# Kernel optimization log

Hardware: AMD Instinct MI355X
Metric: run time of the kernel (lower is better)

Reference implementation:

```python
import jax, jax.numpy as jnp
import numpy as np

B, S, T = 32, 2048, 768
NH, DH, DHID = 8, 96, 384  # num_heads, head_dim, hidden_dim=4*head_dim


def setup_inputs() -> dict:
    key = jax.random.key(0)
    k = jax.random.split(key, 7)
    token_embeddings = jax.random.normal(k[0], (B, S, T), dtype=jnp.float32)
    attention_mask = jnp.ones((B, S), dtype=jnp.float32)
    # per-head Linear params, stacked on a leading head axis (PyTorch default-ish init scale)
    P_w = jax.random.normal(k[1], (NH, T, DH), dtype=jnp.float32) * (1.0 / np.sqrt(T))
    P_b = jax.random.normal(k[2], (NH, DH), dtype=jnp.float32) * 0.01
    W1_w = jax.random.normal(k[3], (NH, DH, DHID), dtype=jnp.float32) * (1.0 / np.sqrt(DH))
    W1_b = jax.random.normal(k[4], (NH, DHID), dtype=jnp.float32) * 0.01
    W2_w = jax.random.normal(k[5], (NH, DHID, DH), dtype=jnp.float32) * (1.0 / np.sqrt(DHID))
    W2_b = jax.random.normal(k[6], (NH, DH), dtype=jnp.float32) * 0.01
    return {
        'token_embeddings': token_embeddings,
        'attention_mask': attention_mask,
        'P_w': P_w, 'P_b': P_b,
        'W1_w': W1_w, 'W1_b': W1_b,
        'W2_w': W2_w, 'W2_b': W2_b,
    }


def reference(token_embeddings, attention_mask, P_w, P_b, W1_w, W1_b, W2_w, W2_b):
    # Batched over heads instead of the original Python loop; same math per head.
    # H_i = P_i(H): (B, NH, S, DH)
    Hi = jnp.einsum('bst,htd->bhsd', token_embeddings, P_w) + P_b[None, :, None, :]
    # A_i = W2_i(relu(W1_i(H_i))): (B, NH, S, DH)
    A = jax.nn.relu(jnp.einsum('bhsd,hde->bhse', Hi, W1_w) + W1_b[None, :, None, :])
    A = jnp.einsum('bhse,hed->bhsd', A, W2_w) + W2_b[None, :, None, :]
    # masked softmax over the sequence axis (log(mask) adds -inf at padded tokens)
    log_mask = jnp.log(attention_mask)[:, None, :, None]  # (B,1,S,1)
    A = jax.nn.softmax(A + log_mask, axis=2)
    # weighted sum over tokens: (B, NH, DH)
    v = jnp.sum(Hi * A, axis=2)
    # concat heads -> (B, NH*DH) == (B, sentence_dim)
    return v.reshape(v.shape[0], NH * DH)
```

## Files before the change

### kernel.cpp

```cpp
#include <hip/hip_runtime.h>
#include <cstdint>
#include <cstddef>

#define Bsz   32
#define Ssz   2048
#define Tsz   768
#define NH    8
#define DH    96
#define DHID  384
#define Ncols (NH*DH)

using u16 = unsigned short;
typedef __bf16 bf16x8 __attribute__((ext_vector_type(8)));
typedef __bf16 bf16x4 __attribute__((ext_vector_type(4)));
typedef float  f32x4  __attribute__((ext_vector_type(4)));

__device__ __forceinline__ u16 f2bn(float f) {
  __bf16 h = (__bf16)f;
  return __builtin_bit_cast(u16, h);
}
__device__ __forceinline__ float b2f(u16 u) {
  return __builtin_bit_cast(float, (uint32_t)u << 16);
}

__global__ __launch_bounds__(256) void k_pack(const float* __restrict__ Pw,
    const float* __restrict__ W1w, const float* __restrict__ W2w,
    u16* __restrict__ B1t, u16* __restrict__ W1t, u16* __restrict__ W2t)
{
  int i = blockIdx.x * 256 + threadIdx.x;
  if (i < 589824) {
    int n = i / 768, k = i % 768;
    int h = n / 96, d = n % 96;
    B1t[i] = f2bn(Pw[(size_t)h*73728 + (size_t)k*96 + d]);
  } else if (i < 589824 + 294912) {
    int j = i - 589824;
    int h = j / 36864, r = j % 36864;
    int n = r / 96, k = r % 96;
    W1t[j] = f2bn(W1w[(size_t)h*36864 + (size_t)k*384 + n]);
  } else if (i < 589824 + 2*294912) {
    int q = i - 589824 - 294912;
    int h = q / 36864, r = q % 36864;
    int n = r / 384, k = r % 384;
    W2t[q] = f2bn(W2w[(size_t)h*36864 + (size_t)k*96 + n]);
  }
}

__global__ __launch_bounds__(256, 2) void k_gemm1(const float* __restrict__ emb,
    const u16* __restrict__ B1t, const float* __restrict__ Pb, u16* __restrict__ Hi)
{
  __shared__ u16 As[256*64];
  __shared__ u16 Bs[128*64];
  const int tid  = threadIdx.x;
  const int lane = tid & 63;
  const int w    = tid >> 6;
  const int wr = w >> 1, wc = w & 1;
  const int L = blockIdx.x;
  const int widx = (L & 7) * 192 + (L >> 3);
  const int bm = widx / 6, bn = widx % 6;
  const int l15 = lane & 15, lg = lane >> 4;

  const int srow   = lane >> 3;
  const int schunk = lane & 7;
  const int wchunk = schunk ^ srow;

  bf16x8 pa[8];
  bf16x8 pb[4];

  auto load_tile = [&](int kt) {
    const int k0 = kt * 64;
    #pragma unroll
    for (int i = 0; i < 8; ++i) {
      const int row = w*64 + i*8 + srow;
      const float* src = emb + (size_t)(bm*256 + row)*Tsz + k0 + schunk*8;
      float4 v0 = *reinterpret_cast<const float4*>(src);
      float4 v1 = *reinterpret_cast<const float4*>(src + 4);
      bf16x8 af;
      af[0] = (__bf16)v0.x; af[1] = (__bf16)v0.y; af[2] = (__bf16)v0.z; af[3] = (__bf16)v0.w;
      af[4] = (__bf16)v1.x; af[5] = (__bf16)v1.y; af[6] = (__bf16)v1.z; af[7] = (__bf16)v1.w;
      pa[i] = af;
    }
    #pragma unroll
    for (int i = 0; i < 4; ++i) {
      const int row = w*32 + i*8 + srow;
      pb[i] = *reinterpret_cast<const bf16x8*>(
          B1t + (size_t)(bn*128 + row)*Tsz + k0 + schunk*8);
    }
  };
  auto write_tile = [&]() {
    #pragma unroll
    for (int i = 0; i < 8; ++i) {
      const int row = w*64 + i*8 + srow;
      *reinterpret_cast<bf16x8*>(&As[row*64 + wchunk*8]) = pa[i];
    }
    #pragma unroll
    for (int i = 0; i < 4; ++i) {
      const int row = w*32 + i*8 + srow;
      *reinterpret_cast<bf16x8*>(&Bs[row*64 + wchunk*8]) = pb[i];
    }
  };

  f32x4 acc[8][4] = {};

  load_tile(0);
  write_tile();
  __syncthreads();

  #pragma unroll 1
  for (int kt = 0; kt < 12; ++kt) {
    if (kt < 11) load_tile(kt + 1);
    #pragma unroll
    for (int kk = 0; kk < 2; ++kk) {
      const int clog = kk*4 + lg;
      bf16x8 b[4];
      #pragma unroll
      for (int c = 0; c < 4; ++c) {
        const int Rb = wc*64 + c*16 + l15;
        b[c] = *reinterpret_cast<const bf16x8*>(&Bs[Rb*64 + (clog ^ (Rb & 7))*8]);
      }
      bf16x8 a[8];
      #pragma unroll
      for (int m = 0; m < 8; ++m) {
        const int R = wr*128 + m*16 + l15;
        a[m] = *reinterpret_cast<const bf16x8*>(&As[R*64 + (clog ^ (R & 7))*8]);
      }
      #pragma unroll
      for (int m = 0; m < 8; ++m)
        #pragma unroll
        for (int c = 0; c < 4; ++c)
          acc[m][c] = __builtin_amdgcn_mfma_f32_16x16x32_bf16(a[m], b[c], acc[m][c], 0, 0, 0);
    }
    __syncthreads();
    if (kt < 11) {
      write_tile();
      __syncthreads();
    }
  }

  #pragma unroll
  for (int c = 0; c < 4; ++c) {
    int col = bn*128 + wc*64 + c*16 + l15;
    float bias = Pb[col];
    #pragma unroll
    for (int m = 0; m < 8; ++m) {
      int row0 = bm*256 + wr*128 + m*16 + lg*4;
      #pragma unroll
      for (int j = 0; j < 4; ++j)
        Hi[(size_t)(row0 + j)*Ncols + col] = f2bn(acc[m][c][j] + bias);
    }
  }
}

__global__ __launch_bounds__(256, 1) void k_ffn_pool(
    const u16* __restrict__ Hi, const u16* __restrict__ W1t, const u16* __restrict__ W2t,
    const float* __restrict__ b1, const float* __restrict__ b2v, const float* __restrict__ mask,
    float* __restrict__ out)
{
  __shared__ u16 W2s[96][392];
  __shared__ u16 Zb[4][2][16][40];
  __shared__ float mb[4][96], lb[4][96], ab[4][96];

  const int tid = threadIdx.x, lane = tid & 63, w = tid >> 6;
  const int l15 = lane & 15, lg = lane >> 4;
  const int h = blockIdx.x, b = blockIdx.y;

  const u16* W1h = W1t + (size_t)h * DHID * DH;
  const u16* W2h = W2t + (size_t)h * DH * DHID;
  const float* b1h = b1 + h * DHID;

  for (int i = tid; i < 96*48; i += 256) {
    int r = i / 48, g = i % 48;
    uint4 v = *reinterpret_cast<const uint4*>(W2h + (size_t)r*DHID + g*8);
    *reinterpret_cast<uint4*>(&W2s[r][g*8]) = v;
  }
  __syncthreads();

  float b2s[6];
  #pragma unroll
  for (int ct = 0; ct < 6; ++ct) b2s[ct] = b2v[h*DH + ct*16 + l15];

  float Mr[6], Lr[6], Ar[6];
  #pragma unroll
  for (int ct = 0; ct < 6; ++ct) { Mr[ct] = -3.4e38f; Lr[ct] = 0.f; Ar[ct] = 0.f; }

  #pragma unroll 1
  for (int pass = 0; pass < 8; ++pass) {
    const size_t prow = (size_t)b*Ssz + (size_t)w*512 + (size_t)pass*64;

    bf16x8 hifr[4][3];
    #pragma unroll
    for (int s = 0; s < 4; ++s)
      #pragma unroll
      for (int ks = 0; ks < 3; ++ks)
        hifr[s][ks] = *reinterpret_cast<const bf16x8*>(
            Hi + (prow + s*16 + l15)*Ncols + h*DH + ks*32 + lg*8);

    f32x4 lgt[4][6] = {};

    #pragma unroll 2
    for (int c = 0; c < 12; ++c) {
      bf16x8 a1c[2][3];
      #pragma unroll
      for (int t = 0; t < 2; ++t)
        #pragma unroll
        for (int ks = 0; ks < 3; ++ks)
          a1c[t][ks] = *reinterpret_cast<const bf16x8*>(
              W1h + (size_t)(c*32 + t*16 + l15)*DH + ks*32 + lg*8);
      float4 bc0 = *reinterpret_cast<const float4*>(b1h + c*32 + lg*4);
      float4 bc1 = *reinterpret_cast<const float4*>(b1h + c*32 + 16 + lg*4);
      bf16x8 b2fr[6];
      #pragma unroll
      for (int ct = 0; ct < 6; ++ct)
        b2fr[ct] = *reinterpret_cast<const bf16x8*>(&W2s[ct*16 + l15][c*32 + lg*8]);

      #pragma unroll
      for (int bi = 0; bi < 2; ++bi) {
        f32x4 z[2][2];
        #pragma unroll
        for (int sl = 0; sl < 2; ++sl) {
          z[sl][0] = f32x4{}; z[sl][1] = f32x4{};
          #pragma unroll
          for (int ks = 0; ks < 3; ++ks) {
            z[sl][0] = __builtin_amdgcn_mfma_f32_16x16x32_bf16(a1c[0][ks], hifr[bi*2+sl][ks], z[sl][0], 0, 0, 0);
            z[sl][1] = __builtin_amdgcn_mfma_f32_16x16x32_bf16(a1c[1][ks], hifr[bi*2+sl][ks], z[sl][1], 0, 0, 0);
          }
        }
        #pragma unroll
        for (int sl = 0; sl < 2; ++sl) {
          bf16x4 p0, p1;
          p0[0] = (__bf16)fmaxf(z[sl][0][0] + bc0.x, 0.f);
          p0[1] = (__bf16)fmaxf(z[sl][0][1] + bc0.y, 0.f);
          p0[2] = (__bf16)fmaxf(z[sl][0][2] + bc0.z, 0.f);
          p0[3] = (__bf16)fmaxf(z[sl][0][3] + bc0.w, 0.f);
          p1[0] = (__bf16)fmaxf(z[sl][1][0] + bc1.x, 0.f);
          p1[1] = (__bf16)fmaxf(z[sl][1][1] + bc1.y, 0.f);
          p1[2] = (__bf16)fmaxf(z[sl][1][2] + bc1.z, 0.f);
          p1[3] = (__bf16)fmaxf(z[sl][1][3] + bc1.w, 0.f);
          *reinterpret_cast<uint2*>(&Zb[w][sl][l15][lg*4])      = __builtin_bit_cast(uint2, p0);
          *reinterpret_cast<uint2*>(&Zb[w][sl][l15][16 + lg*4]) = __builtin_bit_cast(uint2, p1);
        }
        #pragma unroll
        for (int sl = 0; sl < 2; ++sl) {
          bf16x8 zf = *reinterpret_cast<const bf16x8*>(&Zb[w][sl][l15][lg*8]);
          #pragma unroll
          for (int ct = 0; ct < 6; ++ct)
            lgt[bi*2+sl][ct] = __builtin_amdgcn_mfma_f32_16x16x32_bf16(zf, b2fr[ct], lgt[bi*2+sl][ct], 0, 0, 0);
        }
      }
    }

    float lmv[4][4];
    #pragma unroll
    for (int s = 0; s < 4; ++s) {
      float4 mk = *reinterpret_cast<const float4*>(&mask[prow + s*16 + lg*4]);
      lmv[s][0] = __logf(mk.x); lmv[s][1] = __logf(mk.y);
      lmv[s][2] = __logf(mk.z); lmv[s][3] = __logf(mk.w);
    }
    float G[4][6][4];
    #pragma unroll
    for (int s = 0; s < 4; ++s)
      #pragma unroll
      for (int ct = 0; ct < 6; ++ct)
        #pragma unroll
        for (int j = 0; j < 4; ++j)
          G[s][ct][j] = b2f(Hi[(prow + s*16 + lg*4 + j)*Ncols + h*DH + ct*16 + l15]);

    #pragma unroll
    for (int ct = 0; ct < 6; ++ct) {
      float av[4][4];
      float m16 = -3.4e38f;
      #pragma unroll
      for (int s = 0; s < 4; ++s)
        #pragma unroll
        for (int j = 0; j < 4; ++j) {
          av[s][j] = lgt[s][ct][j] + b2s[ct] + lmv[s][j];
          m16 = fmaxf(m16, av[s][j]);
        }
      m16 = fmaxf(m16, __shfl_xor(m16, 16));
      m16 = fmaxf(m16, __shfl_xor(m16, 32));
      float l16 = 0.f, a16 = 0.f;
      #pragma unroll
      for (int s = 0; s < 4; ++s)
        #pragma unroll
        for (int j = 0; j < 4; ++j) {
          float p = __expf(av[s][j] - m16);
          l16 += p;
          a16 += p * G[s][ct][j];
        }
      l16 += __shfl_xor(l16, 16); l16 += __shfl_xor(l16, 32);
      a16 += __shfl_xor(a16, 16); a16 += __shfl_xor(a16, 32);
      float M2 = fmaxf(Mr[ct], m16);
      float eo = __expf(Mr[ct] - M2), en = __expf(m16 - M2);
      Lr[ct] = Lr[ct]*eo + l16*en;
      Ar[ct] = Ar[ct]*eo + a16*en;
      Mr[ct] = M2;
    }
  }

  if (lane < 16) {
    #pragma unroll
    for (int ct = 0; ct < 6; ++ct) {
      mb[w][ct*16 + l15] = Mr[ct];
      lb[w][ct*16 + l15] = Lr[ct];
      ab[w][ct*16 + l15] = Ar[ct];
    }
  }
  __syncthreads();
  if (tid < 96) {
    float m = fmaxf(fmaxf(mb[0][tid], mb[1][tid]), fmaxf(mb[2][tid], mb[3][tid]));
    float l = 0.f, a = 0.f;
    #pragma unroll
    for (int q = 0; q < 4; ++q) {
      float sc = __expf(mb[q][tid] - m);
      l += lb[q][tid] * sc;
      a += ab[q][tid] * sc;
    }
    out[(size_t)b * Ncols + h*DH + tid] = a / l;
  }
}

extern "C" void kernel_launch(void* const* d_in, const int* in_sizes, int n_in,
                              void* d_out, int out_size, void* d_ws, size_t ws_size,
                              hipStream_t stream)
{
  const float* emb  = (const float*)d_in[0];
  const float* mask = (const float*)d_in[1];
  const float* Pw   = (const float*)d_in[2];
  const float* Pb   = (const float*)d_in[3];
  const float* W1w  = (const float*)d_in[4];
  const float* W1b  = (const float*)d_in[5];
  const float* W2w  = (const float*)d_in[6];
  const float* W2b  = (const float*)d_in[7];
  float* out = (float*)d_out;

  char* ws = (char*)d_ws;
  u16*   Hi  = (u16*)(ws);
  u16*   B1t = (u16*)(ws + 100663296ull);
  u16*   W1t = (u16*)(ws + 101842944ull);
  u16*   W2t = (u16*)(ws + 102432768ull);

  k_pack<<<dim3(4608), dim3(256), 0, stream>>>(Pw, W1w, W2w, B1t, W1t, W2t);
  k_gemm1<<<dim3(1536), dim3(256), 0, stream>>>(emb, B1t, Pb, Hi);
  k_ffn_pool<<<dim3(8, 32), dim3(256), 0, stream>>>(Hi, W1t, W2t, W1b, W2b, mask, out);
}
```

Baseline: 274.5 us.

## Widen GEMM1 tile to 256x256 with 512 threads and stage W1 in LDS

The projection GEMM now uses 512-thread blocks covering a 256x256 output tile instead of 256x128, halving the grid and the redundant fp32 embedding reads and conversions per output column. The FFN-pool kernel copies the per-head W1 into shared memory once instead of reloading it from global memory every chunk. It also processes one 16-row slice at a time, shrinking the Zb scratch buffer and reusing it for the final cross-wave softmax merge. The changes raise LDS use and per-block register pressure, and the half-size grid (768 blocks) may leave compute units less evenly loaded.

```diff
diff --git a/kernel.cpp b/kernel.cpp
--- a/kernel.cpp
+++ b/kernel.cpp
@@ -45,32 +45,32 @@
   }
 }
 
-__global__ __launch_bounds__(256, 2) void k_gemm1(const float* __restrict__ emb,
+__global__ __launch_bounds__(512, 1) void k_gemm1(const float* __restrict__ emb,
     const u16* __restrict__ B1t, const float* __restrict__ Pb, u16* __restrict__ Hi)
 {
   __shared__ u16 As[256*64];
-  __shared__ u16 Bs[128*64];
+  __shared__ u16 Bs[256*64];
   const int tid  = threadIdx.x;
   const int lane = tid & 63;
   const int w    = tid >> 6;
-  const int wr = w >> 1, wc = w & 1;
+  const int wr = w >> 2, wc = w & 3;
   const int L = blockIdx.x;
-  const int widx = (L & 7) * 192 + (L >> 3);
-  const int bm = widx / 6, bn = widx % 6;
+  const int widx = (L & 7) * 96 + (L >> 3);
+  const int bm = widx / 3, bn = widx % 3;
   const int l15 = lane & 15, lg = lane >> 4;
 
   const int srow   = lane >> 3;
   const int schunk = lane & 7;
   const int wchunk = schunk ^ srow;
 
-  bf16x8 pa[8];
+  bf16x8 pa[4];
   bf16x8 pb[4];
 
   auto load_tile = [&](int kt) {
     const int k0 = kt * 64;
     #pragma unroll
-    for (int i = 0; i < 8; ++i) {
-      const int row = w*64 + i*8 + srow;
+    for (int i = 0; i < 4; ++i) {
+      const int row = w*32 + i*8 + srow;
       const float* src = emb + (size_t)(bm*256 + row)*Tsz + k0 + schunk*8;
       float4 v0 = *reinterpret_cast<const float4*>(src);
       float4 v1 = *reinterpret_cast<const float4*>(src + 4);
@@ -83,18 +83,14 @@
     for (int i = 0; i < 4; ++i) {
       const int row = w*32 + i*8 + srow;
       pb[i] = *reinterpret_cast<const bf16x8*>(
-          B1t + (size_t)(bn*128 + row)*Tsz + k0 + schunk*8);
+          B1t + (size_t)(bn*256 + row)*Tsz + k0 + schunk*8);
     }
   };
   auto write_tile = [&]() {
     #pragma unroll
-    for (int i = 0; i < 8; ++i) {
-      const int row = w*64 + i*8 + srow;
-      *reinterpret_cast<bf16x8*>(&As[row*64 + wchunk*8]) = pa[i];
-    }
-    #pragma unroll
     for (int i = 0; i < 4; ++i) {
       const int row = w*32 + i*8 + srow;
+      *reinterpret_cast<bf16x8*>(&As[row*64 + wchunk*8]) = pa[i];
       *reinterpret_cast<bf16x8*>(&Bs[row*64 + wchunk*8]) = pb[i];
     }
   };
@@ -138,7 +134,7 @@
 
   #pragma unroll
   for (int c = 0; c < 4; ++c) {
-    int col = bn*128 + wc*64 + c*16 + l15;
+    int col = bn*256 + wc*64 + c*16 + l15;
     float bias = Pb[col];
     #pragma unroll
     for (int m = 0; m < 8; ++m) {
@@ -155,9 +151,9 @@
     const float* __restrict__ b1, const float* __restrict__ b2v, const float* __restrict__ mask,
     float* __restrict__ out)
 {
+  __shared__ u16 W1s[384][104];
   __shared__ u16 W2s[96][392];
-  __shared__ u16 Zb[4][2][16][40];
-  __shared__ float mb[4][96], lb[4][96], ab[4][96];
+  __shared__ u16 Zb[4][16][40];
 
   const int tid = threadIdx.x, lane = tid & 63, w = tid >> 6;
   const int l15 = lane & 15, lg = lane >> 4;
@@ -167,6 +163,11 @@
   const u16* W2h = W2t + (size_t)h * DH * DHID;
   const float* b1h = b1 + h * DHID;
 
+  for (int i = tid; i < 384*12; i += 256) {
+    int r = i / 12, g = i % 12;
+    uint4 v = *reinterpret_cast<const uint4*>(W1h + (size_t)r*DH + g*8);
+    *reinterpret_cast<uint4*>(&W1s[r][g*8]) = v;
+  }
   for (int i = tid; i < 96*48; i += 256) {
     int r = i / 48, g = i % 48;
     uint4 v = *reinterpret_cast<const uint4*>(W2h + (size_t)r*DHID + g*8);
@@ -204,7 +205,7 @@
         #pragma unroll
         for (int ks = 0; ks < 3; ++ks)
           a1c[t][ks] = *reinterpret_cast<const bf16x8*>(
-              W1h + (size_t)(c*32 + t*16 + l15)*DH + ks*32 + lg*8);
+              &W1s[c*32 + t*16 + l15][ks*32 + lg*8]);
       float4 bc0 = *reinterpret_cast<const float4*>(b1h + c*32 + lg*4);
       float4 bc1 = *reinterpret_cast<const float4*>(b1h + c*32 + 16 + lg*4);
       bf16x8 b2fr[6];
@@ -213,38 +214,28 @@
         b2fr[ct] = *reinterpret_cast<const bf16x8*>(&W2s[ct*16 + l15][c*32 + lg*8]);
 
       #pragma unroll
-      for (int bi = 0; bi < 2; ++bi) {
-        f32x4 z[2][2];
-        #pragma unroll
-        for (int sl = 0; sl < 2; ++sl) {
-          z[sl][0] = f32x4{}; z[sl][1] = f32x4{};
-          #pragma unroll
-          for (int ks = 0; ks < 3; ++ks) {
-            z[sl][0] = __builtin_amdgcn_mfma_f32_16x16x32_bf16(a1c[0][ks], hifr[bi*2+sl][ks], z[sl][0], 0, 0, 0);
-            z[sl][1] = __builtin_amdgcn_mfma_f32_16x16x32_bf16(a1c[1][ks], hifr[bi*2+sl][ks], z[sl][1], 0, 0, 0);
-          }
+      for (int s = 0; s < 4; ++s) {
+        f32x4 z0 = {}, z1 = {};
+        #pragma unroll
+        for (int ks = 0; ks < 3; ++ks) {
+          z0 = __builtin_amdgcn_mfma_f32_16x16x32_bf16(a1c[0][ks], hifr[s][ks], z0, 0, 0, 0);
+          z1 = __builtin_amdgcn_mfma_f32_16x16x32_bf16(a1c[1][ks], hifr[s][ks], z1, 0, 0, 0);
         }
-        #pragma unroll
-        for (int sl = 0; sl < 2; ++sl) {
-          bf16x4 p0, p1;
-          p0[0] = (__bf16)fmaxf(z[sl][0][0] + bc0.x, 0.f);
-          p0[1] = (__bf16)fmaxf(z[sl][0][1] + bc0.y, 0.f);
-          p0[2] = (__bf16)fmaxf(z[sl][0][2] + bc0.z, 0.f);
-          p0[3] = (__bf16)fmaxf(z[sl][0][3] + bc0.w, 0.f);
-          p1[0] = (__bf16)fmaxf(z[sl][1][0] + bc1.x, 0.f);
-          p1[1] = (__bf16)fmaxf(z[sl][1][1] + bc1.y, 0.f);
-          p1[2] = (__bf16)fmaxf(z[sl][1][2] + bc1.z, 0.f);
-          p1[3] = (__bf16)fmaxf(z[sl][1][3] + bc1.w, 0.f);
-          *reinterpret_cast<uint2*>(&Zb[w][sl][l15][lg*4])      = __builtin_bit_cast(uint2, p0);
-          *reinterpret_cast<uint2*>(&Zb[w][sl][l15][16 + lg*4]) = __builtin_bit_cast(uint2, p1);
-        }
-        #pragma unroll
-        for (int sl = 0; sl < 2; ++sl) {
-          bf16x8 zf = *reinterpret_cast<const bf16x8*>(&Zb[w][sl][l15][lg*8]);
-          #pragma unroll
-          for (int ct = 0; ct < 6; ++ct)
-            lgt[bi*2+sl][ct] = __builtin_amdgcn_mfma_f32_16x16x32_bf16(zf, b2fr[ct], lgt[bi*2+sl][ct], 0, 0, 0);
-        }
+        bf16x4 p0, p1;
+        p0[0] = (__bf16)fmaxf(z0[0] + bc0.x, 0.f);
+        p0[1] = (__bf16)fmaxf(z0[1] + bc0.y, 0.f);
+        p0[2] = (__bf16)fmaxf(z0[2] + bc0.z, 0.f);
+        p0[3] = (__bf16)fmaxf(z0[3] + bc0.w, 0.f);
+        p1[0] = (__bf16)fmaxf(z1[0] + bc1.x, 0.f);
+        p1[1] = (__bf16)fmaxf(z1[1] + bc1.y, 0.f);
+        p1[2] = (__bf16)fmaxf(z1[2] + bc1.z, 0.f);
+        p1[3] = (__bf16)fmaxf(z1[3] + bc1.w, 0.f);
+        *reinterpret_cast<uint2*>(&Zb[w][l15][lg*4])      = __builtin_bit_cast(uint2, p0);
+        *reinterpret_cast<uint2*>(&Zb[w][l15][16 + lg*4]) = __builtin_bit_cast(uint2, p1);
+        bf16x8 zf = *reinterpret_cast<const bf16x8*>(&Zb[w][l15][lg*8]);
+        #pragma unroll
+        for (int ct = 0; ct < 6; ++ct)
+          lgt[s][ct] = __builtin_amdgcn_mfma_f32_16x16x32_bf16(zf, b2fr[ct], lgt[s][ct], 0, 0, 0);
       }
     }
 
@@ -296,24 +287,26 @@
     }
   }
 
+  float* mw = reinterpret_cast<float*>(&Zb[w][0][0]);
   if (lane < 16) {
     #pragma unroll
     for (int ct = 0; ct < 6; ++ct) {
-      mb[w][ct*16 + l15] = Mr[ct];
-      lb[w][ct*16 + l15] = Lr[ct];
-      ab[w][ct*16 + l15] = Ar[ct];
+      mw[      ct*16 + l15] = Mr[ct];
+      mw[ 96 + ct*16 + l15] = Lr[ct];
+      mw[192 + ct*16 + l15] = Ar[ct];
     }
   }
   __syncthreads();
   if (tid < 96) {
-    float m = fmaxf(fmaxf(mb[0][tid], mb[1][tid]), fmaxf(mb[2][tid], mb[3][tid]));
-    float l = 0.f, a = 0.f;
-    #pragma unroll
-    for (int q = 0; q < 4; ++q) {
-      float sc = __expf(mb[q][tid] - m);
-      l += lb[q][tid] * sc;
-      a += ab[q][tid] * sc;
-    }
+    const float* m0 = reinterpret_cast<const float*>(&Zb[0][0][0]);
+    const float* m1 = reinterpret_cast<const float*>(&Zb[1][0][0]);
+    const float* m2 = reinterpret_cast<const float*>(&Zb[2][0][0]);
+    const float* m3 = reinterpret_cast<const float*>(&Zb[3][0][0]);
+    float m = fmaxf(fmaxf(m0[tid], m1[tid]), fmaxf(m2[tid], m3[tid]));
+    float e0 = __expf(m0[tid] - m), e1 = __expf(m1[tid] - m);
+    float e2 = __expf(m2[tid] - m), e3 = __expf(m3[tid] - m);
+    float l = m0[96+tid]*e0 + m1[96+tid]*e1 + m2[96+tid]*e2 + m3[96+tid]*e3;
+    float a = m0[192+tid]*e0 + m1[192+tid]*e1 + m2[192+tid]*e2 + m3[192+tid]*e3;
     out[(size_t)b * Ncols + h*DH + tid] = a / l;
   }
 }
@@ -339,6 +332,6 @@
   u16*   W2t = (u16*)(ws + 102432768ull);
 
   k_pack<<<dim3(4608), dim3(256), 0, stream>>>(Pw, W1w, W2w, B1t, W1t, W2t);
-  k_gemm1<<<dim3(1536), dim3(256), 0, stream>>>(emb, B1t, Pb, Hi);
+  k_gemm1<<<dim3(768), dim3(512), 0, stream>>>(emb, B1t, Pb, Hi);
   k_ffn_pool<<<dim3(8, 32), dim3(256), 0, stream>>>(Hi, W1t, W2t, W1b, W2b, mask, out);
 }
```

After: 253.5 us. 7.6% less time.
